# Optimization experiments

Hardware: AMD Instinct MI355X
Metric: run time of the kernel (lower is better)

## Reference

```python
import jax, jax.numpy as jnp
import numpy as np
from jax import lax

C = 512   # n_feat == Cn == Cdim (forced by DA_conv/CA_layer consistency)
H, W = 16, 32  # reshape_codebooks(512)
K = 3     # kernel_size
RED = 8   # reduction


def _lrelu(x):
    return jax.nn.leaky_relu(x, 0.1)


def _conv1x1(x, w, b=None):
    # x: (B,C,H,W), w: (O,C) -- torch Conv2d(.,.,1) weight squeezed
    y = jnp.einsum('oc,bchw->bohw', w, x)
    if b is not None:
        y = y + b[None, :, None, None]
    return y


def _conv3x3(x, w, b):
    # x: (B,C,H,W), w: (O,C,3,3) OIHW, padding=k//2 == SAME for odd k
    y = lax.conv_general_dilated(x, w, (1, 1), 'SAME',
                                 dimension_numbers=('NCHW', 'OIHW', 'NCHW'))
    return y + b[None, :, None, None]


def _da_conv(c, deg, kw1, kw2, pw, pb, caw1, caw2):
    # per-channel dynamic kernels from degradation vectors: (Cn, K*K)
    kern = (_lrelu(deg @ kw1.T) @ kw2.T).reshape(C, 1, K, K)
    # depthwise conv, groups = b1*c1 = C (b1 == 1)
    out = lax.conv_general_dilated(c, kern, (1, 1), 'SAME',
                                   feature_group_count=C,
                                   dimension_numbers=('NCHW', 'OIHW', 'NCHW'))
    out = _lrelu(out)
    out = _conv1x1(out, pw, pb)
    # CA_layer: deg reshaped to (1, Cn, 16, 32), channel attention, deg * att
    dr = deg.reshape(1, C, H, W)
    att = jax.nn.sigmoid(_conv1x1(_lrelu(_conv1x1(dr, caw1)), caw2))
    return out + dr * att


def setup_inputs() -> dict:
    key = jax.random.key(0)
    ks = jax.random.split(key, 16)
    n = lambda i, shape, s=0.05: jax.random.normal(ks[i], shape, dtype=jnp.float32) * s
    return dict(
        c=jax.random.normal(ks[0], (1, C, H, W), dtype=jnp.float32),
        deg=jax.random.normal(ks[1], (C, C), dtype=jnp.float32) * 0.1,
        k1_w1=n(2, (C, C)), k1_w2=n(3, (K * K, C)),
        p1_w=n(4, (C, C)), p1_b=jnp.zeros((C,), jnp.float32),
        ca1_w1=n(5, (C // RED, C)), ca1_w2=n(6, (C, C // RED)),
        conv1_w=n(7, (C, C, K, K)), conv1_b=jnp.zeros((C,), jnp.float32),
        k2_w1=n(8, (C, C)), k2_w2=n(9, (K * K, C)),
        p2_w=n(10, (C, C)), p2_b=jnp.zeros((C,), jnp.float32),
        ca2_w1=n(11, (C // RED, C)), ca2_w2=n(12, (C, C // RED)),
        conv2_w=n(13, (C, C, K, K)), conv2_b=jnp.zeros((C,), jnp.float32),
    )


def reference(c, deg, k1_w1, k1_w2, p1_w, p1_b, ca1_w1, ca1_w2,
              conv1_w, conv1_b, k2_w1, k2_w2, p2_w, p2_b,
              ca2_w1, ca2_w2, conv2_w, conv2_b):
    out = _lrelu(_da_conv(c, deg, k1_w1, k1_w2, p1_w, p1_b, ca1_w1, ca1_w2))
    out = _lrelu(_conv3x3(out, conv1_w, conv1_b))
    out = _lrelu(_da_conv(out, deg, k2_w1, k2_w2, p2_w, p2_b, ca2_w1, ca2_w2))
    return _conv3x3(out, conv2_w, conv2_b) + c
```

## Files before the change

kernel.cpp:

```cpp
#include <hip/hip_runtime.h>
#include <hip/hip_bf16.h>

typedef __attribute__((ext_vector_type(8))) unsigned short ushort8;
typedef __attribute__((ext_vector_type(8))) __bf16 bf16x8;
typedef __attribute__((ext_vector_type(4))) float f32x4;
typedef __attribute__((ext_vector_type(4))) unsigned short ushort4v;

__device__ __forceinline__ float lrelu_f(float v){ return v > 0.f ? v : 0.1f*v; }

__device__ __forceinline__ unsigned short f2bf(float v){
  unsigned u = __float_as_uint(v);
  unsigned r = (u + 0x7fffu + ((u>>16)&1u)) >> 16;
  return (unsigned short)r;
}
__device__ __forceinline__ float bf2f(unsigned short u){
  return __uint_as_float(((unsigned)u)<<16);
}

__device__ __forceinline__ void gload16(const void* g, void* l){
  __builtin_amdgcn_global_load_lds(
    (const __attribute__((address_space(1))) unsigned int*)g,
    (__attribute__((address_space(3))) unsigned int*)l, 16, 0, 0);
}

__device__ __forceinline__ void packq(const float* __restrict__ s,
                                      unsigned short* __restrict__ d, int i){
  const float4 v = ((const float4*)s)[i];
  ushort4v o; o.x=f2bf(v.x); o.y=f2bf(v.y); o.z=f2bf(v.z); o.w=f2bf(v.w);
  *(ushort4v*)(d + (size_t)i*4) = o;
}

__global__ __launch_bounds__(256) void k_pack_all(
  const float* __restrict__ k1_w1, const float* __restrict__ k2_w1,
  const float* __restrict__ p1_w,  const float* __restrict__ p2_w,
  const float* __restrict__ ca1_w1,const float* __restrict__ ca1_w2,
  const float* __restrict__ ca2_w1,const float* __restrict__ ca2_w2,
  const float* __restrict__ deg,
  unsigned short* __restrict__ K1B, unsigned short* __restrict__ K2B,
  unsigned short* __restrict__ P1B, unsigned short* __restrict__ P2B,
  unsigned short* __restrict__ CA1A,unsigned short* __restrict__ CA1B,
  unsigned short* __restrict__ CA2A,unsigned short* __restrict__ CA2B,
  unsigned short* __restrict__ DEGB,unsigned short* __restrict__ DEGT){
  int i = blockIdx.x*256 + threadIdx.x;
  if (i < 65536){ packq(k1_w1, K1B, i); return; } i -= 65536;
  if (i < 65536){ packq(k2_w1, K2B, i); return; } i -= 65536;
  if (i < 65536){ packq(p1_w,  P1B, i); return; } i -= 65536;
  if (i < 65536){ packq(p2_w,  P2B, i); return; } i -= 65536;
  if (i < 8192){ packq(ca1_w1, CA1A, i); return; } i -= 8192;
  if (i < 8192){ packq(ca1_w2, CA1B, i); return; } i -= 8192;
  if (i < 8192){ packq(ca2_w1, CA2A, i); return; } i -= 8192;
  if (i < 8192){ packq(ca2_w2, CA2B, i); return; } i -= 8192;
  if (i < 65536){ packq(deg, DEGB, i); return; } i -= 65536;
  if (i < 65536){
    const int j = i*4; const int p = j>>9, c = j&511;
    ushort4v o;
    o.x = f2bf(deg[(size_t)(c+0)*512 + p]);
    o.y = f2bf(deg[(size_t)(c+1)*512 + p]);
    o.z = f2bf(deg[(size_t)(c+2)*512 + p]);
    o.w = f2bf(deg[(size_t)(c+3)*512 + p]);
    *(ushort4v*)(DEGT + (size_t)j) = o;
  }
}

__device__ __forceinline__ void gemm32(
    const unsigned short* __restrict__ A, const unsigned short* __restrict__ Bt,
    int m0, int n0, int K, int tid,
    unsigned short* lA, unsigned short* lB, f32x4& acc){
  const int wid = tid>>6, lane = tid&63;
  const int half = tid>>7, st_ = tid&127;
  const int srow = st_>>2, skb = st_&3;
  const unsigned short* gS = (half ? Bt + (size_t)(n0+srow)*K
                                   : A  + (size_t)(m0+srow)*K);
  unsigned short* lS = half ? lB : lA;
  const int soff0 = srow*64 + 8*(skb ^ (srow&7));
  const int soff1 = srow*64 + 8*((skb+4) ^ (srow&7));

  const int wr = (wid>>1)*16, wc = (wid&1)*16;
  const int l15 = lane&15, lkb = lane>>4;
  int aoff[2], boff[2];
  #pragma unroll
  for (int h=0;h<2;h++){
    const int Ra = wr + l15;
    aoff[h] = Ra*64 + 8*((lkb+4*h) ^ (Ra&7));
    const int Rb = wc + l15;
    boff[h] = Rb*64 + 8*((lkb+4*h) ^ (Rb&7));
  }

  const int nst = K>>6;
  ushort8 r0 = *(const ushort8*)(gS + skb*8);
  ushort8 r1 = *(const ushort8*)(gS + (skb+4)*8);
  *(ushort8*)(lS + soff0) = r0;
  *(ushort8*)(lS + soff1) = r1;
  if (nst > 1){
    r0 = *(const ushort8*)(gS + 64 + skb*8);
    r1 = *(const ushort8*)(gS + 64 + (skb+4)*8);
  }
  __syncthreads();
  for (int st=0; st<nst; ++st){
    const int cur = (st&1)*2048;
    bf16x8 af[2], bf[2];
    #pragma unroll
    for (int h=0;h<2;h++){
      af[h] = *(const bf16x8*)(lA + cur + aoff[h]);
      bf[h] = *(const bf16x8*)(lB + cur + boff[h]);
    }
    if (st+1 < nst){
      const int nxt = ((st+1)&1)*2048;
      *(ushort8*)(lS + nxt + soff0) = r0;
      *(ushort8*)(lS + nxt + soff1) = r1;
      if (st+2 < nst){
        r0 = *(const ushort8*)(gS + (size_t)(st+2)*64 + skb*8);
        r1 = *(const ushort8*)(gS + (size_t)(st+2)*64 + (skb+4)*8);
      }
    }
    #pragma unroll
    for (int h=0;h<2;h++)
      acc = __builtin_amdgcn_mfma_f32_16x16x32_bf16(af[h], bf[h], acc, 0,0,0);
    __syncthreads();
  }
}

__global__ __launch_bounds__(256) void k_mgemm_pre(
    const unsigned short* __restrict__ DEGB, const unsigned short* __restrict__ DEGT,
    const unsigned short* __restrict__ K1B,  const unsigned short* __restrict__ K2B,
    const unsigned short* __restrict__ CA1A, const unsigned short* __restrict__ CA2A,
    const float* __restrict__ conv1_w, const float* __restrict__ conv2_w,
    const float* __restrict__ kw2a, const float* __restrict__ kw2b,
    float* __restrict__ KP1, float* __restrict__ KP2,
    unsigned short* __restrict__ HID1, unsigned short* __restrict__ HID2,
    unsigned short* __restrict__ WB1, unsigned short* __restrict__ WB2){
  const int z = blockIdx.z;
  const int tid = threadIdx.x;
  if (z >= 2 && blockIdx.y >= 2){
    const float* src      = (z==2) ? conv1_w : conv2_w;
    unsigned short* dst   = (z==2) ? WB1 : WB2;
    const int base = (((blockIdx.y-2)*16 + blockIdx.x)*256) + tid;
    for (int i = base; i < 589824; i += 57344){
      const int o_ = i/1152; const int r4 = (i - o_*1152)*4;
      const int t = r4>>9; const int ci = r4&511;
      const float* s = src + (size_t)o_*4608;
      ushort4v o;
      o.x = f2bf(s[(ci+0)*9 + t]); o.y = f2bf(s[(ci+1)*9 + t]);
      o.z = f2bf(s[(ci+2)*9 + t]); o.w = f2bf(s[(ci+3)*9 + t]);
      *(ushort4v*)(dst + (size_t)o_*4608 + r4) = o;
    }
    return;
  }
  __shared__ unsigned short lA[4096], lB[4096];
  __shared__ float kp[2][32][9];
  const int wid = tid>>6, lane = tid&63;
  const int l15 = lane&15, lkb = lane>>4;

  if (z < 2){
    const int it = blockIdx.x, jc = blockIdx.y;
    const unsigned short* Bt = z ? K2B : K1B;
    const float* kw2 = z ? kw2b : kw2a;
    float* KP        = z ? KP2 : KP1;
    const int m0 = it*32, n0 = jc*32;
    f32x4 acc = {};
    gemm32(DEGB, Bt, m0, n0, 512, tid, lA, lB, acc);

    const int wr = (wid>>1)*16, wc2 = wid&1;
    const int col = n0 + wc2*16 + l15;
    float w[9];
    #pragma unroll
    for (int t=0;t<9;t++) w[t] = kw2[t*512 + col];
    #pragma unroll
    for (int r=0;r<4;r++){
      const float v = lrelu_f(acc[r]);
      const int row = wr + lkb*4 + r;
      #pragma unroll
      for (int t=0;t<9;t++){
        float q = v*w[t];
        q += __shfl_xor(q,1); q += __shfl_xor(q,2);
        q += __shfl_xor(q,4); q += __shfl_xor(q,8);
        if (l15==0) kp[wc2][row][t] = q;
      }
    }
    __syncthreads();
    for (int i = tid; i < 288; i += 256){
      const int row = i/9, t = i - row*9;
      KP[((size_t)jc*512 + m0 + row)*9 + t] = kp[0][row][t] + kp[1][row][t];
    }
  } else {
    const unsigned short* caw = (z==2) ? CA1A : CA2A;
    unsigned short* HID = (z==2) ? HID1 : HID2;
    const int m0 = blockIdx.x*32, n0 = blockIdx.y*32;
    f32x4 acc = {};
    gemm32(DEGT, caw, m0, n0, 512, tid, lA, lB, acc);
    const int wr = (wid>>1)*16, wc = (wid&1)*16;
    #pragma unroll
    for (int r=0;r<4;r++){
      const int row = m0 + wr + lkb*4 + r;
      const int col = n0 + wc + l15;
      HID[(size_t)row*64 + col] = f2bf(lrelu_f(acc[r]));
    }
  }
}

__device__ __forceinline__ void gemm64(
    const unsigned short* __restrict__ A, const unsigned short* __restrict__ Bt,
    int m0, int n0, int K, int tid,
    unsigned short* lA, unsigned short* lB, f32x4 acc[2][2]){
  const int wid = tid>>6, lane = tid&63;
  const int srow = tid>>2, skb = tid&3;
  const unsigned short* gA = A  + (size_t)(m0+srow)*K + skb*8;
  const unsigned short* gB = Bt + (size_t)(n0+srow)*K + skb*8;
  const int soff = srow*32 + 8*(skb ^ (srow&3));
  const int wr = (wid>>1)*32, wc = (wid&1)*32;
  const int l15 = lane&15, lkb = lane>>4;
  int aoff[2], boff[2];
  #pragma unroll
  for (int s=0;s<2;s++){
    const int Ra = wr + s*16 + l15;
    aoff[s] = Ra*32 + 8*(lkb ^ (Ra&3));
    const int Rb = wc + s*16 + l15;
    boff[s] = Rb*32 + 8*(lkb ^ (Rb&3));
  }
  const int nst = K>>5;
  ushort8 ra = *(const ushort8*)gA;
  ushort8 rb = *(const ushort8*)gB;
  *(ushort8*)(lA + soff) = ra;
  *(ushort8*)(lB + soff) = rb;
  if (nst > 1){ ra = *(const ushort8*)(gA+32); rb = *(const ushort8*)(gB+32); }
  __syncthreads();
  for (int st=0; st<nst; ++st){
    const int cur = (st&1)*2048;
    bf16x8 af[2], bfr[2];
    #pragma unroll
    for (int s=0;s<2;s++){
      af[s]  = *(const bf16x8*)(lA + cur + aoff[s]);
      bfr[s] = *(const bf16x8*)(lB + cur + boff[s]);
    }
    if (st+1 < nst){
      const int nxt = ((st+1)&1)*2048;
      *(ushort8*)(lA + nxt + soff) = ra;
      *(ushort8*)(lB + nxt + soff) = rb;
      if (st+2 < nst){
        ra = *(const ushort8*)(gA + (size_t)(st+2)*32);
        rb = *(const ushort8*)(gB + (size_t)(st+2)*32);
      }
    }
    #pragma unroll
    for (int mi=0;mi<2;mi++)
      #pragma unroll
      for (int ni=0;ni<2;ni++)
        acc[mi][ni] = __builtin_amdgcn_mfma_f32_16x16x32_bf16(af[mi], bfr[ni], acc[mi][ni], 0,0,0);
    __syncthreads();
  }
}

__global__ __launch_bounds__(256) void k_att_dw(
    const unsigned short* __restrict__ CA1B, const unsigned short* __restrict__ CA2B,
    const unsigned short* __restrict__ HID1, const unsigned short* __restrict__ HID2,
    float* __restrict__ ATT1, float* __restrict__ ATT2,
    const float* __restrict__ xin, const float* __restrict__ KP1,
    unsigned short* __restrict__ DWLT, unsigned short* __restrict__ XTP){
  __shared__ __align__(16) unsigned char smem[16640];
  const int tid = threadIdx.x;
  int bid = blockIdx.x;
  if (bid < 128){
    unsigned short* lA = (unsigned short*)smem;
    unsigned short* lB = lA + 4096;
    const int b = bid>>6, t6 = bid&63;
    const unsigned short* A   = b ? CA2B : CA1B;
    const unsigned short* Bt  = b ? HID2 : HID1;
    float* ATT                = b ? ATT2 : ATT1;
    const int m0 = (t6>>3)*64, n0 = (t6&7)*64;
    f32x4 acc[2][2] = {};
    gemm64(A, Bt, m0, n0, 64, tid, lA, lB, acc);
    const int wid = tid>>6, lane = tid&63;
    const int wr = (wid>>1)*32, wc = (wid&1)*32;
    const int l15 = lane&15, lkb = lane>>4;
    #pragma unroll
    for (int mi=0;mi<2;mi++)
      #pragma unroll
      for (int ni=0;ni<2;ni++){
        const int row = m0 + wr + mi*16 + lkb*4;
        const int col = n0 + wc + ni*16 + l15;
        #pragma unroll
        for (int r=0;r<4;r++)
          ATT[(size_t)(row+r)*512 + col] = 1.f/(1.f + expf(-acc[mi][ni][r]));
      }
  } else {
    bid -= 128;
    const int c = bid;
    {
      const int idx = bid*256 + tid;
      if (idx < 12800){
        const int si = idx>>7, wi = idx&127;
        int slot;
        if (si < 34) slot = si;
        else if (si < 68) slot = 578 + (si-34);
        else if (si < 84) slot = (si-67)*34;
        else slot = (si-83)*34 + 33;
        ushort4v zz = {};
        *(ushort4v*)(XTP + (size_t)slot*512 + wi*4) = zz;
      }
    }
    float* plane = (float*)smem;
    float* ks = plane + 612;
    for (int i=tid;i<612;i+=256) plane[i]=0.f;
    if (tid<9){
      float s=0.f;
      #pragma unroll
      for (int jc=0;jc<16;jc++) s += KP1[((size_t)jc*512 + c)*9 + tid];
      ks[tid]=s;
    }
    #pragma unroll
    for (int q=0;q<2;q++){
      const int px = tid + q*256;
      plane[((px>>5)+1)*34 + (px&31)+1] = xin[(size_t)c*512 + px];
    }
    __syncthreads();
    #pragma unroll
    for (int q=0;q<2;q++){
      const int px = tid + q*256;
      const int iy = px>>5, ix = px&31;
      float s = 0.f;
      #pragma unroll
      for (int dy=0;dy<3;dy++)
        #pragma unroll
        for (int dx=0;dx<3;dx++)
          s += plane[(iy+dy)*34 + ix+dx]*ks[dy*3+dx];
      DWLT[(size_t)px*512 + c] = f2bf(lrelu_f(s));
    }
  }
}

__global__ __launch_bounds__(512) void k_dwconv_red(const unsigned short* __restrict__ part,
    const float* __restrict__ bias, const float* __restrict__ KP,
    unsigned short* __restrict__ yt, int nchunks){
  const int c = blockIdx.x;
  const int p = threadIdx.x;
  const int iy = p>>5, ix = p&31;
  __shared__ float plane[18*34];
  __shared__ float ks[9];
  for (int i=p;i<18*34;i+=512) plane[i]=0.f;
  if (p < 9){
    float s = 0.f;
    #pragma unroll
    for (int jc=0;jc<16;jc++) s += KP[((size_t)jc*512 + c)*9 + p];
    ks[p] = s;
  }
  __syncthreads();
  if (p < 128){
    const float b = bias[c];
    float4 a4 = {b,b,b,b};
    for (int s=0;s<nchunks;s++){
      const ushort4v v = ((const ushort4v*)(part + (size_t)s*262144 + c*512))[p];
      a4.x += bf2f(v.x); a4.y += bf2f(v.y); a4.z += bf2f(v.z); a4.w += bf2f(v.w);
    }
    a4.x = lrelu_f(a4.x); a4.y = lrelu_f(a4.y);
    a4.z = lrelu_f(a4.z); a4.w = lrelu_f(a4.w);
    const int px0 = p*4;
    float* dst = &plane[((px0>>5)+1)*34 + (px0&31)+1];
    dst[0]=a4.x; dst[1]=a4.y; dst[2]=a4.z; dst[3]=a4.w;
  }
  __syncthreads();
  float s = 0.f;
  #pragma unroll
  for (int dy=0;dy<3;dy++)
    #pragma unroll
    for (int dx=0;dx<3;dx++)
      s += plane[(iy+dy)*34 + ix+dx]*ks[dy*3+dx];
  yt[(size_t)p*512 + c] = f2bf(lrelu_f(s));
}

__global__ __launch_bounds__(256) void k_pw(
    const unsigned short* __restrict__ A, const unsigned short* __restrict__ Bt,
    const float* __restrict__ bias,
    const float* __restrict__ E1, const float* __restrict__ E2,
    unsigned short* __restrict__ XTP){
  __shared__ unsigned short lA[4096], lB[4096];
  __shared__ float tile[32][33];
  const int tid = threadIdx.x;
  const int wid = tid>>6, lane = tid&63;
  const int M0 = blockIdx.x*32, N0 = blockIdx.y*32;

  f32x4 acc = {};
  gemm32(A, Bt, M0, N0, 512, tid, lA, lB, acc);

  const int wr = (wid>>1)*16, wc = (wid&1)*16;
  const int l15 = lane&15, lkb = lane>>4;
  #pragma unroll
  for (int r=0;r<4;r++){
    const int rl = wr + lkb*4 + r;
    const int cl = wc + l15;
    const int rr = M0 + rl, col = N0 + cl;
    float v = acc[r] + bias[rr] + E1[(size_t)rr*512+col]*E2[(size_t)rr*512+col];
    tile[rl][cl] = lrelu_f(v);
  }
  __syncthreads();
  const int pr = tid>>3, q = tid&7;
  const int p = N0 + pr;
  const int slot = ((p>>5)+1)*34 + (p&31) + 1;
  ushort4v o;
  o.x = f2bf(tile[q*4+0][pr]); o.y = f2bf(tile[q*4+1][pr]);
  o.z = f2bf(tile[q*4+2][pr]); o.w = f2bf(tile[q*4+3][pr]);
  *(ushort4v*)(XTP + (size_t)slot*512 + M0 + q*4) = o;
}

template<int KCH>
__global__ __launch_bounds__(256) void k_mfma_conv(
    const unsigned short* __restrict__ WB,
    const unsigned short* __restrict__ XTP,
    unsigned short* __restrict__ part){
  __shared__ __attribute__((aligned(16))) unsigned short lA[2][4096];
  __shared__ __attribute__((aligned(16))) unsigned short lB[2][8192];
  const int tid = threadIdx.x;
  const int wid = tid>>6, lane = tid&63;
  const int m0 = blockIdx.x*64, n0 = blockIdx.y*128;
  const int k0 = blockIdx.z*KCH;

  const int wrow = wid*8 + (lane>>3);
  const int clin = lane&7;
  const unsigned short* asrc[2];
  #pragma unroll
  for (int j=0;j<2;j++){
    const int r = j*32 + wrow;
    asrc[j] = WB + (size_t)(m0+r)*4608 + k0 + (clin ^ (r&7))*8;
  }
  int bpy[4], bpx[4], bchk[4];
  #pragma unroll
  for (int j=0;j<4;j++){
    const int r = j*32 + wrow;
    const int pp = n0 + r;
    bpy[j] = pp>>5; bpx[j] = pp&31;
    bchk[j] = (clin ^ (r&7))*8;
  }

  const int wr = (wid>>1)*32, wc = (wid&1)*64;
  const int l15 = lane&15, lkb = lane>>4;
  int aoff[2][2], boff[4][2];
  #pragma unroll
  for (int s=0;s<2;s++){
    const int Ra = wr + s*16 + l15;
    #pragma unroll
    for (int h=0;h<2;h++) aoff[s][h] = Ra*64 + 8*((lkb+4*h) ^ (Ra&7));
  }
  #pragma unroll
  for (int u=0;u<4;u++){
    const int Rb = wc + u*16 + l15;
    #pragma unroll
    for (int h=0;h<2;h++) boff[u][h] = Rb*64 + 8*((lkb+4*h) ^ (Rb&7));
  }

  auto stage = [&](int buf, int st){
    #pragma unroll
    for (int j=0;j<2;j++)
      gload16(asrc[j] + st*64, &lA[buf][j*2048 + wid*512]);
    const int k = k0 + st*64;
    const int t = k>>9;
    const int dy = t/3, dx = t - dy*3;
    const int kc = k & 511;
    #pragma unroll
    for (int j=0;j<4;j++){
      const int slot = (bpy[j]+dy)*34 + bpx[j]+dx;
      gload16(XTP + (size_t)slot*512 + kc + bchk[j],
              &lB[buf][j*2048 + wid*512]);
    }
  };

  constexpr int NST = KCH/64;
  f32x4 acc[2][4] = {};
  stage(0, 0);
  __syncthreads();
  #pragma unroll
  for (int st=0; st<NST; ++st){
    const int cur = st&1;
    if (st+1 < NST) stage(cur^1, st+1);
    bf16x8 af[2][2], bfr[4][2];
    #pragma unroll
    for (int s=0;s<2;s++)
      #pragma unroll
      for (int h=0;h<2;h++) af[s][h] = *(const bf16x8*)(&lA[cur][aoff[s][h]]);
    #pragma unroll
    for (int u=0;u<4;u++)
      #pragma unroll
      for (int h=0;h<2;h++) bfr[u][h] = *(const bf16x8*)(&lB[cur][boff[u][h]]);
    #pragma unroll
    for (int h=0;h<2;h++)
      #pragma unroll
      for (int s=0;s<2;s++)
        #pragma unroll
        for (int u=0;u<4;u++)
          acc[s][u] = __builtin_amdgcn_mfma_f32_16x16x32_bf16(af[s][h], bfr[u][h], acc[s][u], 0,0,0);
    __syncthreads();
  }

  unsigned short* pbase = part + (size_t)blockIdx.z*262144;
  #pragma unroll
  for (int s=0;s<2;s++)
    #pragma unroll
    for (int u=0;u<4;u++){
      const int row = m0 + wr + s*16 + lkb*4;
      const int col = n0 + wc + u*16 + l15;
      #pragma unroll
      for (int r=0;r<4;r++)
        pbase[(size_t)(row+r)*512 + col] = f2bf(acc[s][u][r]);
    }
}

__global__ __launch_bounds__(256) void k_reduce_final(const unsigned short* __restrict__ part,
    const float* __restrict__ bias, const float* __restrict__ res,
    float* __restrict__ y, int nchunks){
  const int i = blockIdx.x*256 + threadIdx.x;
  const int o = i>>7;
  const float b = bias[o];
  float4 a4 = {b,b,b,b};
  for (int s=0;s<nchunks;s++){
    const ushort4v v = ((const ushort4v*)part)[(size_t)s*65536 + i];
    a4.x += bf2f(v.x); a4.y += bf2f(v.y); a4.z += bf2f(v.z); a4.w += bf2f(v.w);
  }
  const float4 rv = ((const float4*)res)[i];
  a4.x += rv.x; a4.y += rv.y; a4.z += rv.z; a4.w += rv.w;
  ((float4*)y)[i] = a4;
}

extern "C" void kernel_launch(void* const* d_in, const int* in_sizes, int n_in,
                              void* d_out, int out_size, void* d_ws, size_t ws_size,
                              hipStream_t stream) {
  (void)in_sizes; (void)n_in; (void)out_size; (void)ws_size;
  const float* xin    = (const float*)d_in[0];
  const float* deg    = (const float*)d_in[1];
  const float* k1_w1  = (const float*)d_in[2];
  const float* k1_w2  = (const float*)d_in[3];
  const float* p1_w   = (const float*)d_in[4];
  const float* p1_b   = (const float*)d_in[5];
  const float* ca1_w1 = (const float*)d_in[6];
  const float* ca1_w2 = (const float*)d_in[7];
  const float* conv1_w= (const float*)d_in[8];
  const float* conv1_b= (const float*)d_in[9];
  const float* k2_w1  = (const float*)d_in[10];
  const float* k2_w2  = (const float*)d_in[11];
  const float* p2_w   = (const float*)d_in[12];
  const float* p2_b   = (const float*)d_in[13];
  const float* ca2_w1 = (const float*)d_in[14];
  const float* ca2_w2 = (const float*)d_in[15];
  const float* conv2_w= (const float*)d_in[16];
  const float* conv2_b= (const float*)d_in[17];
  float* out = (float*)d_out;

  const int NS = 18;

  float* ws = (float*)d_ws;
  unsigned short* PART = (unsigned short*)ws;
  ws += (size_t)NS*131072;
  unsigned short* HID1 = PART;
  unsigned short* HID2 = HID1 + 32768;
  float* KP1  = ws;  ws += 73728;
  float* KP2  = ws;  ws += 73728;
  float* ATT1 = ws;  ws += 262144;
  float* ATT2 = ws;  ws += 262144;
  unsigned short* DEGB = (unsigned short*)ws; ws += 131072;
  unsigned short* DEGT = (unsigned short*)ws; ws += 131072;
  unsigned short* K1B  = (unsigned short*)ws; ws += 131072;
  unsigned short* K2B  = (unsigned short*)ws; ws += 131072;
  unsigned short* XTP  = K1B;
  unsigned short* P1B  = (unsigned short*)ws; ws += 131072;
  unsigned short* P2B  = (unsigned short*)ws; ws += 131072;
  unsigned short* CA1A = (unsigned short*)ws; ws += 16384;
  unsigned short* CA1B = (unsigned short*)ws; ws += 16384;
  unsigned short* CA2A = (unsigned short*)ws; ws += 16384;
  unsigned short* CA2B = (unsigned short*)ws; ws += 16384;
  unsigned short* DWLT = (unsigned short*)ws; ws += 131072;
  unsigned short* WB1  = (unsigned short*)ws; ws += 1179648;
  unsigned short* WB2  = (unsigned short*)ws; ws += 1179648;

  k_pack_all<<<1664,256,0,stream>>>(k1_w1,k2_w1,p1_w,p2_w,
      ca1_w1,ca1_w2,ca2_w1,ca2_w2, deg,
      K1B,K2B,P1B,P2B, CA1A,CA1B,CA2A,CA2B, DEGB,DEGT);

  k_mgemm_pre<<<dim3(16,16,4),256,0,stream>>>(DEGB,DEGT, K1B,K2B, CA1A,CA2A,
      conv1_w, conv2_w, k1_w2, k2_w2, KP1,KP2, HID1,HID2, WB1,WB2);

  k_att_dw<<<640,256,0,stream>>>(CA1B,CA2B, HID1,HID2, ATT1,ATT2,
      xin, KP1, DWLT, XTP);

  k_pw<<<dim3(16,16),256,0,stream>>>(P1B, DWLT, p1_b, deg, ATT1, XTP);
  k_mfma_conv<256><<<dim3(8,4,18),256,0,stream>>>(WB1, XTP, PART);
  k_dwconv_red<<<512,512,0,stream>>>(PART, conv1_b, KP2, DWLT, NS);
  k_pw<<<dim3(16,16),256,0,stream>>>(P2B, DWLT, p2_b, deg, ATT2, XTP);
  k_mfma_conv<256><<<dim3(8,4,18),256,0,stream>>>(WB2, XTP, PART);
  k_reduce_final<<<256,256,0,stream>>>(PART, conv2_b, xin, out, NS);
}
```

Measured before the change: 75.94 us.

## Fuse channel-attention GEMM and sigmoid into pointwise conv epilogue

Channel-attention logits are no longer computed by the k_att_dw kernel and written to ATT1/ATT2 as fp32 buffers. Each k_pw block now runs a second small K=64 GEMM (CA weights × hidden) into a separate accumulator and applies the sigmoid in its epilogue, multiplying by deg directly. This removes the 2×1MB fp32 attention write and read traffic and shrinks the first kernel to just the depthwise conv. The cost is extra MFMA work and LDS reuse inside k_pw. HID buffers also move from aliasing PART to dedicated workspace.

```diff
diff --git a/kernel.cpp b/kernel.cpp
--- a/kernel.cpp
+++ b/kernel.cpp
@@ -198,133 +198,50 @@
   }
 }
 
-__device__ __forceinline__ void gemm64(
-    const unsigned short* __restrict__ A, const unsigned short* __restrict__ Bt,
-    int m0, int n0, int K, int tid,
-    unsigned short* lA, unsigned short* lB, f32x4 acc[2][2]){
-  const int wid = tid>>6, lane = tid&63;
-  const int srow = tid>>2, skb = tid&3;
-  const unsigned short* gA = A  + (size_t)(m0+srow)*K + skb*8;
-  const unsigned short* gB = Bt + (size_t)(n0+srow)*K + skb*8;
-  const int soff = srow*32 + 8*(skb ^ (srow&3));
-  const int wr = (wid>>1)*32, wc = (wid&1)*32;
-  const int l15 = lane&15, lkb = lane>>4;
-  int aoff[2], boff[2];
-  #pragma unroll
-  for (int s=0;s<2;s++){
-    const int Ra = wr + s*16 + l15;
-    aoff[s] = Ra*32 + 8*(lkb ^ (Ra&3));
-    const int Rb = wc + s*16 + l15;
-    boff[s] = Rb*32 + 8*(lkb ^ (Rb&3));
-  }
-  const int nst = K>>5;
-  ushort8 ra = *(const ushort8*)gA;
-  ushort8 rb = *(const ushort8*)gB;
-  *(ushort8*)(lA + soff) = ra;
-  *(ushort8*)(lB + soff) = rb;
-  if (nst > 1){ ra = *(const ushort8*)(gA+32); rb = *(const ushort8*)(gB+32); }
-  __syncthreads();
-  for (int st=0; st<nst; ++st){
-    const int cur = (st&1)*2048;
-    bf16x8 af[2], bfr[2];
-    #pragma unroll
-    for (int s=0;s<2;s++){
-      af[s]  = *(const bf16x8*)(lA + cur + aoff[s]);
-      bfr[s] = *(const bf16x8*)(lB + cur + boff[s]);
-    }
-    if (st+1 < nst){
-      const int nxt = ((st+1)&1)*2048;
-      *(ushort8*)(lA + nxt + soff) = ra;
-      *(ushort8*)(lB + nxt + soff) = rb;
-      if (st+2 < nst){
-        ra = *(const ushort8*)(gA + (size_t)(st+2)*32);
-        rb = *(const ushort8*)(gB + (size_t)(st+2)*32);
-      }
-    }
-    #pragma unroll
-    for (int mi=0;mi<2;mi++)
-      #pragma unroll
-      for (int ni=0;ni<2;ni++)
-        acc[mi][ni] = __builtin_amdgcn_mfma_f32_16x16x32_bf16(af[mi], bfr[ni], acc[mi][ni], 0,0,0);
-    __syncthreads();
-  }
-}
-
-__global__ __launch_bounds__(256) void k_att_dw(
-    const unsigned short* __restrict__ CA1B, const unsigned short* __restrict__ CA2B,
-    const unsigned short* __restrict__ HID1, const unsigned short* __restrict__ HID2,
-    float* __restrict__ ATT1, float* __restrict__ ATT2,
+__global__ __launch_bounds__(256) void k_dw1(
     const float* __restrict__ xin, const float* __restrict__ KP1,
     unsigned short* __restrict__ DWLT, unsigned short* __restrict__ XTP){
-  __shared__ __align__(16) unsigned char smem[16640];
+  __shared__ float plane[612];
+  __shared__ float ks[9];
   const int tid = threadIdx.x;
-  int bid = blockIdx.x;
-  if (bid < 128){
-    unsigned short* lA = (unsigned short*)smem;
-    unsigned short* lB = lA + 4096;
-    const int b = bid>>6, t6 = bid&63;
-    const unsigned short* A   = b ? CA2B : CA1B;
-    const unsigned short* Bt  = b ? HID2 : HID1;
-    float* ATT                = b ? ATT2 : ATT1;
-    const int m0 = (t6>>3)*64, n0 = (t6&7)*64;
-    f32x4 acc[2][2] = {};
-    gemm64(A, Bt, m0, n0, 64, tid, lA, lB, acc);
-    const int wid = tid>>6, lane = tid&63;
-    const int wr = (wid>>1)*32, wc = (wid&1)*32;
-    const int l15 = lane&15, lkb = lane>>4;
-    #pragma unroll
-    for (int mi=0;mi<2;mi++)
+  const int c = blockIdx.x;
+  {
+    const int idx = blockIdx.x*256 + tid;
+    if (idx < 12800){
+      const int si = idx>>7, wi = idx&127;
+      int slot;
+      if (si < 34) slot = si;
+      else if (si < 68) slot = 578 + (si-34);
+      else if (si < 84) slot = (si-67)*34;
+      else slot = (si-83)*34 + 33;
+      ushort4v zz = {};
+      *(ushort4v*)(XTP + (size_t)slot*512 + wi*4) = zz;
+    }
+  }
+  for (int i=tid;i<612;i+=256) plane[i]=0.f;
+  if (tid<9){
+    float s=0.f;
+    #pragma unroll
+    for (int jc=0;jc<16;jc++) s += KP1[((size_t)jc*512 + c)*9 + tid];
+    ks[tid]=s;
+  }
+  #pragma unroll
+  for (int q=0;q<2;q++){
+    const int px = tid + q*256;
+    plane[((px>>5)+1)*34 + (px&31)+1] = xin[(size_t)c*512 + px];
+  }
+  __syncthreads();
+  #pragma unroll
+  for (int q=0;q<2;q++){
+    const int px = tid + q*256;
+    const int iy = px>>5, ix = px&31;
+    float s = 0.f;
+    #pragma unroll
+    for (int dy=0;dy<3;dy++)
       #pragma unroll
-      for (int ni=0;ni<2;ni++){
-        const int row = m0 + wr + mi*16 + lkb*4;
-        const int col = n0 + wc + ni*16 + l15;
-        #pragma unroll
-        for (int r=0;r<4;r++)
-          ATT[(size_t)(row+r)*512 + col] = 1.f/(1.f + expf(-acc[mi][ni][r]));
-      }
-  } else {
-    bid -= 128;
-    const int c = bid;
-    {
-      const int idx = bid*256 + tid;
-      if (idx < 12800){
-        const int si = idx>>7, wi = idx&127;
-        int slot;
-        if (si < 34) slot = si;
-        else if (si < 68) slot = 578 + (si-34);
-        else if (si < 84) slot = (si-67)*34;
-        else slot = (si-83)*34 + 33;
-        ushort4v zz = {};
-        *(ushort4v*)(XTP + (size_t)slot*512 + wi*4) = zz;
-      }
-    }
-    float* plane = (float*)smem;
-    float* ks = plane + 612;
-    for (int i=tid;i<612;i+=256) plane[i]=0.f;
-    if (tid<9){
-      float s=0.f;
-      #pragma unroll
-      for (int jc=0;jc<16;jc++) s += KP1[((size_t)jc*512 + c)*9 + tid];
-      ks[tid]=s;
-    }
-    #pragma unroll
-    for (int q=0;q<2;q++){
-      const int px = tid + q*256;
-      plane[((px>>5)+1)*34 + (px&31)+1] = xin[(size_t)c*512 + px];
-    }
-    __syncthreads();
-    #pragma unroll
-    for (int q=0;q<2;q++){
-      const int px = tid + q*256;
-      const int iy = px>>5, ix = px&31;
-      float s = 0.f;
-      #pragma unroll
-      for (int dy=0;dy<3;dy++)
-        #pragma unroll
-        for (int dx=0;dx<3;dx++)
-          s += plane[(iy+dy)*34 + ix+dx]*ks[dy*3+dx];
-      DWLT[(size_t)px*512 + c] = f2bf(lrelu_f(s));
-    }
+      for (int dx=0;dx<3;dx++)
+        s += plane[(iy+dy)*34 + ix+dx]*ks[dy*3+dx];
+    DWLT[(size_t)px*512 + c] = f2bf(lrelu_f(s));
   }
 }
 
@@ -369,8 +286,8 @@
 
 __global__ __launch_bounds__(256) void k_pw(
     const unsigned short* __restrict__ A, const unsigned short* __restrict__ Bt,
-    const float* __restrict__ bias,
-    const float* __restrict__ E1, const float* __restrict__ E2,
+    const unsigned short* __restrict__ CAB, const unsigned short* __restrict__ HID,
+    const float* __restrict__ bias, const float* __restrict__ deg,
     unsigned short* __restrict__ XTP){
   __shared__ unsigned short lA[4096], lB[4096];
   __shared__ float tile[32][33];
@@ -380,6 +297,8 @@
 
   f32x4 acc = {};
   gemm32(A, Bt, M0, N0, 512, tid, lA, lB, acc);
+  f32x4 att = {};
+  gemm32(CAB, HID, M0, N0, 64, tid, lA, lB, att);
 
   const int wr = (wid>>1)*16, wc = (wid&1)*16;
   const int l15 = lane&15, lkb = lane>>4;
@@ -388,7 +307,8 @@
     const int rl = wr + lkb*4 + r;
     const int cl = wc + l15;
     const int rr = M0 + rl, col = N0 + cl;
-    float v = acc[r] + bias[rr] + E1[(size_t)rr*512+col]*E2[(size_t)rr*512+col];
+    const float a = 1.f/(1.f + expf(-att[r]));
+    float v = acc[r] + bias[rr] + deg[(size_t)rr*512+col]*a;
     tile[rl][cl] = lrelu_f(v);
   }
   __syncthreads();
@@ -547,12 +467,10 @@
   float* ws = (float*)d_ws;
   unsigned short* PART = (unsigned short*)ws;
   ws += (size_t)NS*131072;
-  unsigned short* HID1 = PART;
-  unsigned short* HID2 = HID1 + 32768;
   float* KP1  = ws;  ws += 73728;
   float* KP2  = ws;  ws += 73728;
-  float* ATT1 = ws;  ws += 262144;
-  float* ATT2 = ws;  ws += 262144;
+  unsigned short* HID1 = (unsigned short*)ws; ws += 16384;
+  unsigned short* HID2 = (unsigned short*)ws; ws += 16384;
   unsigned short* DEGB = (unsigned short*)ws; ws += 131072;
   unsigned short* DEGT = (unsigned short*)ws; ws += 131072;
   unsigned short* K1B  = (unsigned short*)ws; ws += 131072;
@@ -575,13 +493,12 @@
   k_mgemm_pre<<<dim3(16,16,4),256,0,stream>>>(DEGB,DEGT, K1B,K2B, CA1A,CA2A,
       conv1_w, conv2_w, k1_w2, k2_w2, KP1,KP2, HID1,HID2, WB1,WB2);
 
-  k_att_dw<<<640,256,0,stream>>>(CA1B,CA2B, HID1,HID2, ATT1,ATT2,
-      xin, KP1, DWLT, XTP);
-
-  k_pw<<<dim3(16,16),256,0,stream>>>(P1B, DWLT, p1_b, deg, ATT1, XTP);
+  k_dw1<<<512,256,0,stream>>>(xin, KP1, DWLT, XTP);
+
+  k_pw<<<dim3(16,16),256,0,stream>>>(P1B, DWLT, CA1B, HID1, p1_b, deg, XTP);
   k_mfma_conv<256><<<dim3(8,4,18),256,0,stream>>>(WB1, XTP, PART);
   k_dwconv_red<<<512,512,0,stream>>>(PART, conv1_b, KP2, DWLT, NS);
-  k_pw<<<dim3(16,16),256,0,stream>>>(P2B, DWLT, p2_b, deg, ATT2, XTP);
+  k_pw<<<dim3(16,16),256,0,stream>>>(P2B, DWLT, CA2B, HID2, p2_b, deg, XTP);
   k_mfma_conv<256><<<dim3(8,4,18),256,0,stream>>>(WB2, XTP, PART);
   k_reduce_final<<<256,256,0,stream>>>(PART, conv2_b, xin, out, NS);
 }
```

Result: no change. 76.22 us (+0.4%).
